# Kernel tuning notes

Measured on AMD Instinct MI355X. Metric: run time of the kernel, lower is better.

Reference implementation:

```python
import jax, jax.numpy as jnp
import numpy as np

B, N, D = 32, 4096, 256
NC, NTPC, NVPT, NS = 16, 8, 4, 16
NT = NC * NTPC          # 128 type codes
NV = NT * NVPT          # 512 variant codes
THRESH = 0.1            # code_sparsity


def setup_inputs() -> dict:
    key = jax.random.key(0)
    ks = jax.random.split(key, 24)
    rn = lambda k, s, sc=0.02: jax.random.normal(k, s, jnp.float32) * sc
    return {
        "X": jax.random.normal(ks[0], (B, N, D), jnp.float32),
        "positions": jax.random.normal(ks[1], (B, N, D), jnp.float32),
        "mask": jnp.ones((B, N), jnp.bool_),
        "category_codes": rn(ks[2], (NC, D)),
        "type_codes": rn(ks[3], (NT, D)),
        "variant_codes": rn(ks[4], (NV, D)),
        "spatial_codes": rn(ks[5], (NS, D)),
        "log_tau": jnp.zeros((1,), jnp.float32),
        "Wk": rn(ks[6], (D, D)), "bk": jnp.zeros((D,), jnp.float32),
        "Wcat": rn(ks[7], (D, D)), "bcat": jnp.zeros((D,), jnp.float32),
        "Wtype": rn(ks[8], (D, D)), "btype": jnp.zeros((D,), jnp.float32),
        "Wvar": rn(ks[9], (D, D)), "bvar": jnp.zeros((D,), jnp.float32),
        "Wsp": rn(ks[10], (D, D)), "bsp": jnp.zeros((D,), jnp.float32),
        "Wg1": rn(ks[11], (D, 2 * D)), "bg1": jnp.zeros((D,), jnp.float32),
        "Wg2": rn(ks[12], (D, D)), "bg2": jnp.zeros((D,), jnp.float32),
        "Wo": rn(ks[13], (D, D)), "bo": jnp.zeros((D,), jnp.float32),
        "ln_g": jnp.ones((D,), jnp.float32), "ln_b": jnp.zeros((D,), jnp.float32),
        "level_weights": jnp.ones((4,), jnp.float32) / 4.0,
    }


def _sparsify(w, thr):
    w = jnp.where(w > thr, w, 0.0)
    return w / (w.sum(-1, keepdims=True) + 1e-8)


def reference(X, positions, mask, category_codes, type_codes, variant_codes,
              spatial_codes, log_tau, Wk, bk, Wcat, bcat, Wtype, btype,
              Wvar, bvar, Wsp, bsp, Wg1, bg1, Wg2, bg2, Wo, bo, ln_g, ln_b,
              level_weights):
    d = X.shape[-1]
    tau = jnp.clip(jnp.exp(log_tau) + 0.1, 0.1, 2.0)  # (1,)
    mv = jnp.finfo(X.dtype).min / 2
    K = X @ Wk.T + bk  # (B,N,d)

    def level(codes, Wq, bq):
        Q = codes @ Wq.T + bq                                    # (M,d)
        attn = jnp.einsum('md,bnd->bmn', Q, K) / jnp.sqrt(jnp.float32(d))
        attn = jnp.where(mask[:, None, :], attn, mv)
        attn = jnp.clip(attn, -50.0, 50.0)
        G = jnp.nan_to_num(jax.nn.softmax(attn, axis=-1))
        H = jnp.einsum('bmn,bnd->bmd', G, X)                     # (B,M,d)
        w_raw = jnp.linalg.norm(H, axis=-1) / tau                # (B,M)
        return H, w_raw

    # level 0: category
    H_cat, w_cat_raw = level(category_codes, Wcat, bcat)
    w_cat_sparse = _sparsify(jax.nn.softmax(w_cat_raw, -1), THRESH)
    # level 1: type (gated by category)
    H_type, w_type_raw = level(type_codes, Wtype, btype)
    w_type_g = (w_type_raw.reshape(-1, NC, NTPC) * w_cat_sparse[:, :, None]).reshape(-1, NT)
    w_type_sparse = _sparsify(jax.nn.softmax(w_type_g, -1), THRESH / 2)
    # level 2: variant (gated by type)
    H_var, w_var_raw = level(variant_codes, Wvar, bvar)
    w_type_exp = jnp.repeat(w_type_sparse, NVPT, axis=-1)        # (B,NV)
    w_var_sparse = _sparsify(jax.nn.softmax(w_var_raw * w_type_exp, -1), THRESH / 4)
    # spatial (independent)
    H_sp, w_sp_raw = level(spatial_codes, Wsp, bsp)
    w_sp_sparse = _sparsify(jax.nn.softmax(w_sp_raw, -1), THRESH)

    z_cat = jnp.einsum('bm,bmd->bd', w_cat_sparse, H_cat)
    z_type = jnp.einsum('bm,bmd->bd', w_type_sparse, H_type)
    z_var = jnp.einsum('bm,bmd->bd', w_var_sparse, H_var)
    z_sp = jnp.einsum('bm,bmd->bd', w_sp_sparse, H_sp)

    lw = jax.nn.softmax(level_weights)
    z = lw[0] * z_cat + lw[1] * z_type + lw[2] * z_var + lw[3] * z_sp

    # position gate: masked mean-pooled positions -> sigmoid gate
    m = mask.astype(X.dtype)
    pos_pool = (positions * m[:, :, None]).sum(1) / (m.sum(1, keepdims=True) + 1e-8)
    h = jax.nn.gelu(jnp.concatenate([z, pos_pool], -1) @ Wg1.T + bg1, approximate=False)
    gate = jax.nn.sigmoid(h @ Wg2.T + bg2)
    z = z * gate

    # out_proj: Linear + LayerNorm
    y = z @ Wo.T + bo
    mu = y.mean(-1, keepdims=True)
    var = ((y - mu) ** 2).mean(-1, keepdims=True)
    y = (y - mu) / jnp.sqrt(var + 1e-5) * ln_g + ln_b
    return y
```

## Files before the change

### kernel.cpp

```cpp
#include <hip/hip_runtime.h>

typedef unsigned short u16;
typedef short v8s __attribute__((ext_vector_type(8)));
typedef float v4f __attribute__((ext_vector_type(4)));

union U16x8 { uint4 u4; v8s s8; u16 us[8]; };

__device__ __forceinline__ u16 f2bf(float x) {
  unsigned int u = __float_as_uint(x);
  u += 0x7fffu + ((u >> 16) & 1u);
  return (u16)(u >> 16);
}

#define GLOBAL_AS __attribute__((address_space(1)))
#define LDS_AS __attribute__((address_space(3)))
__device__ __forceinline__ void async16(const void* g, void* l) {
  __builtin_amdgcn_global_load_lds((const GLOBAL_AS unsigned int*)g,
                                   (LDS_AS unsigned int*)l, 16, 0, 0);
}

#define BB 32
#define NN 4096
#define DD 256
#define M_TOT 672
#define M_PAD 704
#define MT_PER_B 11
#define NSPLIT 4
#define NCHUNK (NN / NSPLIT)

__global__ void kz_zero(float* __restrict__ p, int n) {
  int i = blockIdx.x * 256 + threadIdx.x;
  if (i < n) p[i] = 0.f;
}

__global__ void k0_q(const float* __restrict__ cat, const float* __restrict__ typ,
                     const float* __restrict__ var, const float* __restrict__ spc,
                     const float* __restrict__ Wcat, const float* __restrict__ bcat,
                     const float* __restrict__ Wtype, const float* __restrict__ btype,
                     const float* __restrict__ Wvar, const float* __restrict__ bvar,
                     const float* __restrict__ Wsp, const float* __restrict__ bsp,
                     float* __restrict__ Qall) {
  __shared__ float cl[DD];
  const int m = blockIdx.x, tid = threadIdx.x;
  const float* codes = nullptr; const float* W = nullptr; const float* bia = nullptr; int r = 0;
  if (m < 16)       { codes = cat; r = m;       W = Wcat;  bia = bcat; }
  else if (m < 144) { codes = typ; r = m - 16;  W = Wtype; bia = btype; }
  else if (m < 656) { codes = var; r = m - 144; W = Wvar;  bia = bvar; }
  else if (m < 672) { codes = spc; r = m - 656; W = Wsp;   bia = bsp; }
  cl[tid] = (m < M_TOT) ? codes[r * DD + tid] : 0.f;
  __syncthreads();
  if (m < M_TOT) {
    float acc = bia[tid];
    const float4* w4 = (const float4*)(W + (size_t)tid * DD);
    const float4* c4 = (const float4*)cl;
    #pragma unroll 8
    for (int k = 0; k < 64; ++k) {
      float4 a = c4[k], b = w4[k];
      acc += a.x * b.x + a.y * b.y + a.z * b.z + a.w * b.w;
    }
    Qall[m * DD + tid] = acc;
  } else {
    Qall[m * DD + tid] = 0.f;
  }
}

__global__ void k1_qp(const float* __restrict__ Qall, const float* __restrict__ Wk,
                      const float* __restrict__ bk, u16* __restrict__ Qp,
                      float* __restrict__ qbw) {
  __shared__ float ql[DD];
  __shared__ float red[4];
  const int m = blockIdx.x, tid = threadIdx.x;
  ql[tid] = Qall[m * DD + tid];
  __syncthreads();
  float acc = 0.f;
  for (int j = 0; j < DD; ++j) acc += ql[j] * Wk[(size_t)j * DD + tid];
  Qp[m * DD + tid] = f2bf(acc);
  float p = ql[tid] * bk[tid];
  #pragma unroll
  for (int off = 32; off > 0; off >>= 1) p += __shfl_down(p, off, 64);
  if ((tid & 63) == 0) red[tid >> 6] = p;
  __syncthreads();
  if (tid == 0) qbw[m] = red[0] + red[1] + red[2] + red[3];
}

__global__ void k2_cast(const float* __restrict__ X, u16* __restrict__ Xb,
                        u16* __restrict__ XbT) {
  __shared__ u16 tl[64][72];
  const int n0 = blockIdx.x * 64, d0 = blockIdx.y * 64, b = blockIdx.z;
  const int tid = threadIdx.x;
  const int nl = tid >> 4, d4 = tid & 15;
  #pragma unroll
  for (int rr = 0; rr < 4; ++rr) {
    const int n = n0 + nl + rr * 16;
    float4 v = *(const float4*)(X + ((size_t)b * NN + n) * DD + d0 + d4 * 4);
    ushort4 h;
    h.x = f2bf(v.x); h.y = f2bf(v.y); h.z = f2bf(v.z); h.w = f2bf(v.w);
    *(ushort4*)(Xb + ((size_t)b * NN + n) * DD + d0 +
                (((d4 >> 1) ^ (n & 7)) << 3) + (d4 & 1) * 4) = h;
    *(ushort4*)(&tl[nl + rr * 16][d4 * 4]) = h;
  }
  __syncthreads();
  const int dl = tid >> 4, n4 = tid & 15;
  #pragma unroll
  for (int rr = 0; rr < 4; ++rr) {
    const int d = dl + rr * 16;
    ushort4 h;
    h.x = tl[n4 * 4 + 0][d]; h.y = tl[n4 * 4 + 1][d];
    h.z = tl[n4 * 4 + 2][d]; h.w = tl[n4 * 4 + 3][d];
    *(ushort4*)(XbT + ((size_t)b * DD + d0 + d) * NN + n0 +
                (((n4 >> 1) ^ (dl & 7)) << 3) + (n4 & 1) * 4) = h;
  }
}

__global__ __launch_bounds__(256, 2) void pf_fused(
    const u16* __restrict__ Xb, const u16* __restrict__ XbT,
    const u16* __restrict__ Qp, const float* __restrict__ qbw,
    const unsigned char* __restrict__ mask,
    float* __restrict__ HP, float* __restrict__ sumsP) {
  __shared__ u16 sX[64 * 256];
  __shared__ u16 sXT[256 * 64];
  __shared__ u16 sP[64 * 64];

  const int id = blockIdx.x;
  const int xcd = id & 7, lin = id >> 3;
  const int ggl = lin / MT_PER_B, k = lin - ggl * MT_PER_B;
  const int gg = xcd * 16 + ggl;
  const int b = gg >> 2, split = gg & 3;
  const int m0 = k * 64;
  const int ns0 = split * NCHUNK;

  const int tid = threadIdx.x;
  const int lane = tid & 63, w = tid >> 6;
  const int q = lane >> 4, c16 = lane & 15;
  const int wmQ = (w >> 1) * 32, wn = (w & 1) * 32;
  const int wd = w * 64;

  v8s aq[2][4][2];
  #pragma unroll
  for (int mi = 0; mi < 2; ++mi) {
    const u16* qrow = Qp + (size_t)(m0 + wmQ + mi * 16 + c16) * DD;
    #pragma unroll
    for (int ks = 0; ks < 4; ++ks)
      #pragma unroll
      for (int kk = 0; kk < 2; ++kk) {
        U16x8 u; u.u4 = *(const uint4*)(qrow + ks * 64 + kk * 32 + q * 8);
        aq[mi][ks][kk] = u.s8;
      }
  }
  float qv[2][4];
  #pragma unroll
  for (int mi = 0; mi < 2; ++mi)
    #pragma unroll
    for (int r = 0; r < 4; ++r)
      qv[mi][r] = qbw[m0 + wmQ + mi * 16 + q * 4 + r];

  v4f hacc[4][4];
  #pragma unroll
  for (int mi = 0; mi < 4; ++mi)
    #pragma unroll
    for (int di = 0; di < 4; ++di) hacc[mi][di] = (v4f){0.f, 0.f, 0.f, 0.f};
  float rs[2][4];
  #pragma unroll
  for (int mi = 0; mi < 2; ++mi)
    #pragma unroll
    for (int r = 0; r < 4; ++r) rs[mi][r] = 0.f;

  const u16* XbB = Xb + (size_t)b * NN * DD;
  const u16* XTB = XbT + (size_t)b * DD * NN;
  const unsigned char* mkB = mask + (size_t)b * NN;

  for (int it = 0; it < NCHUNK / 64; ++it) {
    const int n0g = ns0 + it * 64;
    __syncthreads();
    #pragma unroll
    for (int i = 0; i < 8; ++i) {
      const int c = i * 256 + tid;
      async16(XbB + (size_t)(n0g + (c >> 5)) * DD + (c & 31) * 8, sX + c * 8);
    }
    #pragma unroll
    for (int i = 0; i < 8; ++i) {
      const int c = i * 256 + tid;
      async16(XTB + (size_t)(c >> 3) * NN + n0g + (c & 7) * 8, sXT + c * 8);
    }
    __syncthreads();

    v4f sacc[2][2];
    #pragma unroll
    for (int mi = 0; mi < 2; ++mi)
      #pragma unroll
      for (int ni = 0; ni < 2; ++ni) sacc[mi][ni] = (v4f){0.f, 0.f, 0.f, 0.f};
    #pragma unroll
    for (int ks = 0; ks < 4; ++ks)
      #pragma unroll
      for (int kk = 0; kk < 2; ++kk) {
        v8s bq[2];
        #pragma unroll
        for (int ni = 0; ni < 2; ++ni) {
          const int n = wn + ni * 16 + c16;
          U16x8 u;
          u.u4 = *(const uint4*)(sX + n * 256 + (((ks * 8 + kk * 4 + q) ^ (n & 7)) << 3));
          bq[ni] = u.s8;
        }
        #pragma unroll
        for (int mi = 0; mi < 2; ++mi)
          #pragma unroll
          for (int ni = 0; ni < 2; ++ni)
            sacc[mi][ni] = __builtin_amdgcn_mfma_f32_16x16x32_bf16(
                aq[mi][ks][kk], bq[ni], sacc[mi][ni], 0, 0, 0);
      }

    #pragma unroll
    for (int ni = 0; ni < 2; ++ni) {
      const int nl = wn + ni * 16 + c16;
      const bool mk = mkB[n0g + nl] != 0;
      #pragma unroll
      for (int mi = 0; mi < 2; ++mi)
        #pragma unroll
        for (int r = 0; r < 4; ++r) {
          float s = (sacc[mi][ni][r] + qv[mi][r]) * 0.0625f;
          s = fminf(fmaxf(s, -50.f), 50.f);
          s = mk ? s : -50.f;
          float p = __expf(s);
          rs[mi][r] += p;
          const int ml = wmQ + mi * 16 + q * 4 + r;
          sP[ml * 64 + (nl ^ ((ml & 7) << 3))] = f2bf(p);
        }
    }
    __syncthreads();

    #pragma unroll
    for (int kk = 0; kk < 2; ++kk) {
      v8s pa[4];
      #pragma unroll
      for (int mi = 0; mi < 4; ++mi) {
        const int ml = mi * 16 + c16;
        U16x8 u;
        u.u4 = *(const uint4*)(sP + ml * 64 + ((kk * 32 + q * 8) ^ ((ml & 7) << 3)));
        pa[mi] = u.s8;
      }
      #pragma unroll
      for (int di = 0; di < 4; ++di) {
        const int d = wd + di * 16 + c16;
        U16x8 u;
        u.u4 = *(const uint4*)(sXT + d * 64 + (((kk * 4 + q) ^ (d & 7)) << 3));
        #pragma unroll
        for (int mi = 0; mi < 4; ++mi)
          hacc[mi][di] = __builtin_amdgcn_mfma_f32_16x16x32_bf16(
              pa[mi], u.s8, hacc[mi][di], 0, 0, 0);
      }
    }
  }

  float* HPb = HP + ((size_t)split * BB + b) * M_PAD * DD;
  #pragma unroll
  for (int mi = 0; mi < 4; ++mi)
    #pragma unroll
    for (int di = 0; di < 4; ++di)
      #pragma unroll
      for (int r = 0; r < 4; ++r) {
        const int m = m0 + mi * 16 + q * 4 + r;
        HPb[(size_t)m * DD + wd + di * 16 + c16] = hacc[mi][di][r];
      }

  __syncthreads();
  float* fred = (float*)sP;
  #pragma unroll
  for (int mi = 0; mi < 2; ++mi)
    #pragma unroll
    for (int r = 0; r < 4; ++r) {
      float v = rs[mi][r];
      v += __shfl_xor(v, 1, 64);
      v += __shfl_xor(v, 2, 64);
      v += __shfl_xor(v, 4, 64);
      v += __shfl_xor(v, 8, 64);
      if (c16 == 0) fred[(w & 1) * 64 + wmQ + mi * 16 + q * 4 + r] = v;
    }
  __syncthreads();
  if (tid < 64) {
    sumsP[((size_t)split * BB + b) * M_PAD + m0 + tid] = fred[tid] + fred[64 + tid];
  }
}

__global__ void khr_reduce(float* __restrict__ HP, const float* __restrict__ sumsP,
                           float* __restrict__ sums, float* __restrict__ nrm) {
  __shared__ float red[64][4];
  const int mt = blockIdx.x, b = blockIdx.y, tid = threadIdx.x;
  const int lane = tid & 63, w = tid >> 6;
  const int m0 = mt * 64;
  const size_t SP = (size_t)BB * M_PAD * DD;
  float* base = HP + ((size_t)b * M_PAD + m0) * DD;
  for (int mi = 0; mi < 64; ++mi) {
    const size_t idx = (size_t)mi * DD + tid;
    float h = base[idx] + base[idx + SP] + base[idx + 2 * SP] + base[idx + 3 * SP];
    base[idx] = h;
    float v = h * h;
    v += __shfl_xor(v, 1, 64);
    v += __shfl_xor(v, 2, 64);
    v += __shfl_xor(v, 4, 64);
    v += __shfl_xor(v, 8, 64);
    v += __shfl_xor(v, 16, 64);
    v += __shfl_xor(v, 32, 64);
    if (lane == 0) red[mi][w] = v;
  }
  __syncthreads();
  if (tid < 64) {
    const size_t o = (size_t)b * M_PAD + m0 + tid;
    nrm[o] = red[tid][0] + red[tid][1] + red[tid][2] + red[tid][3];
    const size_t ss = (size_t)BB * M_PAD;
    const size_t si = (size_t)b * M_PAD + m0 + tid;
    sums[o] = sumsP[si] + sumsP[si + ss] + sumsP[si + 2 * ss] + sumsP[si + 3 * ss];
  }
}

__global__ void k4_pool(const float* __restrict__ pos, const unsigned char* __restrict__ mask,
                        float* __restrict__ pp, float* __restrict__ cnt) {
  __shared__ float sp[4][256];
  __shared__ float sc[4];
  const int cx = blockIdx.x, b = blockIdx.y, tid = threadIdx.x;
  const int nl = tid >> 6, d4 = tid & 63;
  const int n0 = cx * 256;
  float4 acc = {0.f, 0.f, 0.f, 0.f};
  float c = 0.f;
  for (int i = 0; i < 64; ++i) {
    const int n = n0 + i * 4 + nl;
    const float m = mask[(size_t)b * NN + n] ? 1.f : 0.f;
    c += m;
    float4 v = *(const float4*)(pos + ((size_t)b * NN + n) * DD + d4 * 4);
    acc.x += m * v.x; acc.y += m * v.y; acc.z += m * v.z; acc.w += m * v.w;
  }
  *(float4*)(&sp[nl][d4 * 4]) = acc;
  if (d4 == 0) sc[nl] = c;
  __syncthreads();
  pp[((size_t)b * 16 + cx) * DD + tid] = sp[0][tid] + sp[1][tid] + sp[2][tid] + sp[3][tid];
  if (tid == 0) cnt[b * 16 + cx] = sc[0] + sc[1] + sc[2] + sc[3];
}

__device__ void softmax_sparsify(const float* in, int nn, float* outp, float thr) {
  float mx = -3.4e38f;
  for (int i = 0; i < nn; ++i) mx = fmaxf(mx, in[i]);
  float s = 0.f;
  for (int i = 0; i < nn; ++i) { float e = __expf(in[i] - mx); outp[i] = e; s += e; }
  float s2 = 0.f;
  for (int i = 0; i < nn; ++i) {
    float v = outp[i] / s;
    v = (v > thr) ? v : 0.f;
    outp[i] = v; s2 += v;
  }
  const float inv = 1.f / (s2 + 1e-8f);
  for (int i = 0; i < nn; ++i) outp[i] *= inv;
}

__global__ void k5a_weights(const float* __restrict__ nrm, const float* __restrict__ sums,
                            const float* __restrict__ log_tau,
                            const float* __restrict__ lvlw, float* __restrict__ wbufG) {
  __shared__ float wr[M_TOT];
  __shared__ float wcat[16], wtyp[128], wvar[512], wsp[16], lw[4];
  __shared__ float tmp[128];
  const int b = blockIdx.x, tid = threadIdx.x;
  const float tau = fminf(fmaxf(__expf(log_tau[0]) + 0.1f, 0.1f), 2.0f);
  for (int m = tid; m < M_TOT; m += 256)
    wr[m] = sqrtf(nrm[(size_t)b * M_PAD + m]) / (sums[(size_t)b * M_PAD + m] * tau);
  __syncthreads();
  if (tid == 0) {
    softmax_sparsify(wr, 16, wcat, 0.1f);
    for (int i = 0; i < 128; ++i) tmp[i] = wr[16 + i] * wcat[i >> 3];
    softmax_sparsify(tmp, 128, wtyp, 0.05f);
    for (int i = 0; i < 512; ++i) wvar[i] = wr[144 + i] * wtyp[i >> 2];
    softmax_sparsify(wvar, 512, wvar, 0.025f);
    softmax_sparsify(wr + 656, 16, wsp, 0.1f);
    float mx = fmaxf(fmaxf(lvlw[0], lvlw[1]), fmaxf(lvlw[2], lvlw[3]));
    float s = 0.f;
    for (int i = 0; i < 4; ++i) { lw[i] = __expf(lvlw[i] - mx); s += lw[i]; }
    for (int i = 0; i < 4; ++i) lw[i] /= s;
  }
  __syncthreads();
  for (int m = tid; m < M_TOT; m += 256) {
    float v;
    if (m < 16)       v = lw[0] * wcat[m];
    else if (m < 144) v = lw[1] * wtyp[m - 16];
    else if (m < 656) v = lw[2] * wvar[m - 144];
    else              v = lw[3] * wsp[m - 656];
    wbufG[(size_t)b * M_PAD + m] = v / sums[(size_t)b * M_PAD + m];
  }
}

__global__ void k5b_z(const float* __restrict__ Hws, const float* __restrict__ wbufG,
                      float* __restrict__ zacc) {
  const int mc = blockIdx.x, b = blockIdx.y, tid = threadIdx.x;
  const float* Hb = Hws + (size_t)b * M_PAD * DD;
  const float* wb = wbufG + (size_t)b * M_PAD;
  float acc = 0.f;
  #pragma unroll 4
  for (int i = 0; i < 84; ++i) {
    const int m = mc * 84 + i;
    acc += wb[m] * Hb[(size_t)m * DD + tid];
  }
  atomicAdd(&zacc[(size_t)b * DD + tid], acc);
}

__global__ void k5c_mlp(const float* __restrict__ zacc, const float* __restrict__ pp,
                        const float* __restrict__ cnt,
                        const float* __restrict__ Wg1, const float* __restrict__ bg1,
                        const float* __restrict__ Wg2, const float* __restrict__ bg2,
                        const float* __restrict__ Wo, const float* __restrict__ bo,
                        const float* __restrict__ lng, const float* __restrict__ lnb,
                        float* __restrict__ out) {
  __shared__ float zb[DD], pb[DD], hb[DD], zg[DD];
  __shared__ float red[8];
  const int b = blockIdx.x, tid = threadIdx.x;
  const int lane = tid & 63, w = tid >> 6;

  float p = 0.f, c = 0.f;
  for (int ch = 0; ch < 16; ++ch) {
    p += pp[((size_t)b * 16 + ch) * DD + tid];
    c += cnt[b * 16 + ch];
  }
  zb[tid] = zacc[(size_t)b * DD + tid];
  pb[tid] = p / (c + 1e-8f);
  __syncthreads();

  float h = bg1[tid];
  {
    const float4* w4 = (const float4*)(Wg1 + (size_t)tid * 512);
    const float4* z4 = (const float4*)zb;
    const float4* p4 = (const float4*)pb;
    for (int k = 0; k < 64; ++k) {
      float4 a = z4[k], bb = w4[k];
      h += a.x * bb.x + a.y * bb.y + a.z * bb.z + a.w * bb.w;
    }
    for (int k = 0; k < 64; ++k) {
      float4 a = p4[k], bb = w4[64 + k];
      h += a.x * bb.x + a.y * bb.y + a.z * bb.z + a.w * bb.w;
    }
  }
  h = 0.5f * h * (1.f + erff(h * 0.70710678118654752f));
  hb[tid] = h;
  __syncthreads();

  float g = bg2[tid];
  {
    const float4* w4 = (const float4*)(Wg2 + (size_t)tid * DD);
    const float4* h4 = (const float4*)hb;
    for (int k = 0; k < 64; ++k) {
      float4 a = h4[k], bb = w4[k];
      g += a.x * bb.x + a.y * bb.y + a.z * bb.z + a.w * bb.w;
    }
  }
  g = 1.f / (1.f + __expf(-g));
  zg[tid] = zb[tid] * g;
  __syncthreads();

  float y = bo[tid];
  {
    const float4* w4 = (const float4*)(Wo + (size_t)tid * DD);
    const float4* z4 = (const float4*)zg;
    for (int k = 0; k < 64; ++k) {
      float4 a = z4[k], bb = w4[k];
      y += a.x * bb.x + a.y * bb.y + a.z * bb.z + a.w * bb.w;
    }
  }

  float s = y;
  #pragma unroll
  for (int off = 32; off > 0; off >>= 1) s += __shfl_xor(s, off, 64);
  if (lane == 0) red[w] = s;
  __syncthreads();
  const float mu = (red[0] + red[1] + red[2] + red[3]) * (1.f / 256.f);
  float dv = (y - mu) * (y - mu);
  #pragma unroll
  for (int off = 32; off > 0; off >>= 1) dv += __shfl_xor(dv, off, 64);
  if (lane == 0) red[4 + w] = dv;
  __syncthreads();
  const float var = (red[4] + red[5] + red[6] + red[7]) * (1.f / 256.f);
  out[(size_t)b * DD + tid] = (y - mu) / sqrtf(var + 1e-5f) * lng[tid] + lnb[tid];
}

extern "C" void kernel_launch(void* const* d_in, const int* in_sizes, int n_in,
                              void* d_out, int out_size, void* d_ws, size_t ws_size,
                              hipStream_t stream) {
  const float* X          = (const float*)d_in[0];
  const float* positions  = (const float*)d_in[1];
  const unsigned char* mask = (const unsigned char*)d_in[2];
  const float* cat  = (const float*)d_in[3];
  const float* typ  = (const float*)d_in[4];
  const float* var  = (const float*)d_in[5];
  const float* spc  = (const float*)d_in[6];
  const float* log_tau = (const float*)d_in[7];
  const float* Wk   = (const float*)d_in[8];   const float* bk    = (const float*)d_in[9];
  const float* Wcat = (const float*)d_in[10];  const float* bcat  = (const float*)d_in[11];
  const float* Wtype= (const float*)d_in[12];  const float* btype = (const float*)d_in[13];
  const float* Wvar = (const float*)d_in[14];  const float* bvar  = (const float*)d_in[15];
  const float* Wsp  = (const float*)d_in[16];  const float* bsp   = (const float*)d_in[17];
  const float* Wg1  = (const float*)d_in[18];  const float* bg1   = (const float*)d_in[19];
  const float* Wg2  = (const float*)d_in[20];  const float* bg2   = (const float*)d_in[21];
  const float* Wo   = (const float*)d_in[22];  const float* bo    = (const float*)d_in[23];
  const float* lng  = (const float*)d_in[24];  const float* lnb   = (const float*)d_in[25];
  const float* lvlw = (const float*)d_in[26];

  char* ws = (char*)d_ws;
  size_t off = 0;
  auto alloc = [&](size_t bytes) { size_t o = off; off = (off + bytes + 255) & ~255ULL; return o; };
  const size_t oXb   = alloc((size_t)BB * NN * DD * 2);
  const size_t oXT   = alloc((size_t)BB * DD * NN * 2);
  const size_t oQall = alloc((size_t)M_PAD * DD * 4);
  const size_t oQp   = alloc((size_t)M_PAD * DD * 2);
  const size_t oQb   = alloc((size_t)M_PAD * 4);
  const size_t oSums = alloc((size_t)BB * M_PAD * 4);
  const size_t oSumsP= alloc((size_t)NSPLIT * BB * M_PAD * 4);
  const size_t oNrm  = alloc((size_t)BB * M_PAD * 4);
  const size_t oZac  = alloc((size_t)BB * DD * 4);
  const size_t oWbf  = alloc((size_t)BB * M_PAD * 4);
  const size_t oHP   = alloc((size_t)NSPLIT * BB * M_PAD * DD * 4);
  const size_t oPP   = alloc((size_t)BB * 16 * DD * 4);
  const size_t oCNT  = alloc((size_t)BB * 16 * 4);

  u16*   Xb   = (u16*)(ws + oXb);
  u16*   XbT  = (u16*)(ws + oXT);
  float* Qall = (float*)(ws + oQall);
  u16*   Qp   = (u16*)(ws + oQp);
  float* qbw  = (float*)(ws + oQb);
  float* sums = (float*)(ws + oSums);
  float* sumsP= (float*)(ws + oSumsP);
  float* nrm  = (float*)(ws + oNrm);
  float* zacc = (float*)(ws + oZac);
  float* wbfG = (float*)(ws + oWbf);
  float* HP   = (float*)(ws + oHP);
  float* ppw  = (float*)(ws + oPP);
  float* cntw = (float*)(ws + oCNT);

  const int nzero = BB * DD;
  kz_zero<<<(nzero + 255) / 256, 256, 0, stream>>>(zacc, nzero);
  k0_q<<<M_PAD, 256, 0, stream>>>(cat, typ, var, spc, Wcat, bcat, Wtype, btype,
                                  Wvar, bvar, Wsp, bsp, Qall);
  k1_qp<<<M_PAD, 256, 0, stream>>>(Qall, Wk, bk, Qp, qbw);
  k2_cast<<<dim3(64, 4, 32), 256, 0, stream>>>(X, Xb, XbT);
  k4_pool<<<dim3(16, 32), 256, 0, stream>>>(positions, mask, ppw, cntw);
  pf_fused<<<dim3(BB * MT_PER_B * NSPLIT), 256, 0, stream>>>(Xb, XbT, Qp, qbw, mask,
                                                             HP, sumsP);
  khr_reduce<<<dim3(MT_PER_B, BB), 256, 0, stream>>>(HP, sumsP, sums, nrm);
  k5a_weights<<<32, 256, 0, stream>>>(nrm, sums, log_tau, lvlw, wbfG);
  k5b_z<<<dim3(8, 32), 256, 0, stream>>>(HP, wbfG, zacc);
  k5c_mlp<<<32, 256, 0, stream>>>(zacc, ppw, cntw, Wg1, bg1, Wg2, bg2, Wo, bo,
                                  lng, lnb, (float*)d_out);
}
```

Before: 736.3 us.

## Register-prefetch next X tile in main kernel, fuse Q kernels, drop z atomics

The main attention kernel stops using direct global-to-LDS async loads. It now loads the next 64-row X and X-transposed tiles into registers while the current tile is computed, then writes them to LDS at the start of the next iteration. Separately, the two query-projection kernels are merged into one so the Qall buffer round trip goes away. The zero-init kernel and the atomic z accumulation are replaced by per-chunk partial sums that the MLP kernel adds up. The register prefetch adds 16 uint4 registers per thread, which may reduce occupancy of a kernel that already holds large accumulator arrays.

```diff
diff --git a/kernel.cpp b/kernel.cpp
--- a/kernel.cpp
+++ b/kernel.cpp
@@ -10,13 +10,6 @@
   unsigned int u = __float_as_uint(x);
   u += 0x7fffu + ((u >> 16) & 1u);
   return (u16)(u >> 16);
-}
-
-#define GLOBAL_AS __attribute__((address_space(1)))
-#define LDS_AS __attribute__((address_space(3)))
-__device__ __forceinline__ void async16(const void* g, void* l) {
-  __builtin_amdgcn_global_load_lds((const GLOBAL_AS unsigned int*)g,
-                                   (LDS_AS unsigned int*)l, 16, 0, 0);
 }
 
 #define BB 32
@@ -28,19 +21,17 @@
 #define NSPLIT 4
 #define NCHUNK (NN / NSPLIT)
 
-__global__ void kz_zero(float* __restrict__ p, int n) {
-  int i = blockIdx.x * 256 + threadIdx.x;
-  if (i < n) p[i] = 0.f;
-}
-
-__global__ void k0_q(const float* __restrict__ cat, const float* __restrict__ typ,
-                     const float* __restrict__ var, const float* __restrict__ spc,
-                     const float* __restrict__ Wcat, const float* __restrict__ bcat,
-                     const float* __restrict__ Wtype, const float* __restrict__ btype,
-                     const float* __restrict__ Wvar, const float* __restrict__ bvar,
-                     const float* __restrict__ Wsp, const float* __restrict__ bsp,
-                     float* __restrict__ Qall) {
+__global__ void k01_q(const float* __restrict__ cat, const float* __restrict__ typ,
+                      const float* __restrict__ var, const float* __restrict__ spc,
+                      const float* __restrict__ Wcat, const float* __restrict__ bcat,
+                      const float* __restrict__ Wtype, const float* __restrict__ btype,
+                      const float* __restrict__ Wvar, const float* __restrict__ bvar,
+                      const float* __restrict__ Wsp, const float* __restrict__ bsp,
+                      const float* __restrict__ Wk, const float* __restrict__ bk,
+                      u16* __restrict__ Qp, float* __restrict__ qbw) {
   __shared__ float cl[DD];
+  __shared__ float ql[DD];
+  __shared__ float red[4];
   const int m = blockIdx.x, tid = threadIdx.x;
   const float* codes = nullptr; const float* W = nullptr; const float* bia = nullptr; int r = 0;
   if (m < 16)       { codes = cat; r = m;       W = Wcat;  bia = bcat; }
@@ -49,8 +40,9 @@
   else if (m < 672) { codes = spc; r = m - 656; W = Wsp;   bia = bsp; }
   cl[tid] = (m < M_TOT) ? codes[r * DD + tid] : 0.f;
   __syncthreads();
+  float acc = 0.f;
   if (m < M_TOT) {
-    float acc = bia[tid];
+    acc = bia[tid];
     const float4* w4 = (const float4*)(W + (size_t)tid * DD);
     const float4* c4 = (const float4*)cl;
     #pragma unroll 8
@@ -58,23 +50,12 @@
       float4 a = c4[k], b = w4[k];
       acc += a.x * b.x + a.y * b.y + a.z * b.z + a.w * b.w;
     }
-    Qall[m * DD + tid] = acc;
-  } else {
-    Qall[m * DD + tid] = 0.f;
-  }
-}
-
-__global__ void k1_qp(const float* __restrict__ Qall, const float* __restrict__ Wk,
-                      const float* __restrict__ bk, u16* __restrict__ Qp,
-                      float* __restrict__ qbw) {
-  __shared__ float ql[DD];
-  __shared__ float red[4];
-  const int m = blockIdx.x, tid = threadIdx.x;
-  ql[tid] = Qall[m * DD + tid];
-  __syncthreads();
-  float acc = 0.f;
-  for (int j = 0; j < DD; ++j) acc += ql[j] * Wk[(size_t)j * DD + tid];
-  Qp[m * DD + tid] = f2bf(acc);
+  }
+  ql[tid] = acc;
+  __syncthreads();
+  float acc2 = 0.f;
+  for (int j = 0; j < DD; ++j) acc2 += ql[j] * Wk[(size_t)j * DD + tid];
+  Qp[m * DD + tid] = f2bf(acc2);
   float p = ql[tid] * bk[tid];
   #pragma unroll
   for (int off = 32; off > 0; off >>= 1) p += __shfl_down(p, off, 64);
@@ -135,6 +116,21 @@
   const int wmQ = (w >> 1) * 32, wn = (w & 1) * 32;
   const int wd = w * 64;
 
+  const u16* XbB = Xb + (size_t)b * NN * DD;
+  const u16* XTB = XbT + (size_t)b * DD * NN;
+  const unsigned char* mkB = mask + (size_t)b * NN;
+
+  uint4 rx[8], rt[8];
+  {
+    const int n0g = ns0;
+    #pragma unroll
+    for (int i = 0; i < 8; ++i) {
+      const int c = i * 256 + tid;
+      rx[i] = *(const uint4*)(XbB + (size_t)(n0g + (c >> 5)) * DD + (c & 31) * 8);
+      rt[i] = *(const uint4*)(XTB + (size_t)(c >> 3) * NN + n0g + (c & 7) * 8);
+    }
+  }
+
   v8s aq[2][4][2];
   #pragma unroll
   for (int mi = 0; mi < 2; ++mi) {
@@ -165,22 +161,23 @@
     #pragma unroll
     for (int r = 0; r < 4; ++r) rs[mi][r] = 0.f;
 
-  const u16* XbB = Xb + (size_t)b * NN * DD;
-  const u16* XTB = XbT + (size_t)b * DD * NN;
-  const unsigned char* mkB = mask + (size_t)b * NN;
-
   for (int it = 0; it < NCHUNK / 64; ++it) {
     const int n0g = ns0 + it * 64;
     __syncthreads();
     #pragma unroll
     for (int i = 0; i < 8; ++i) {
       const int c = i * 256 + tid;
-      async16(XbB + (size_t)(n0g + (c >> 5)) * DD + (c & 31) * 8, sX + c * 8);
-    }
-    #pragma unroll
-    for (int i = 0; i < 8; ++i) {
-      const int c = i * 256 + tid;
-      async16(XTB + (size_t)(c >> 3) * NN + n0g + (c & 7) * 8, sXT + c * 8);
+      *(uint4*)(sX + c * 8) = rx[i];
+      *(uint4*)(sXT + c * 8) = rt[i];
+    }
+    if (it < NCHUNK / 64 - 1) {
+      const int n1g = n0g + 64;
+      #pragma unroll
+      for (int i = 0; i < 8; ++i) {
+        const int c = i * 256 + tid;
+        rx[i] = *(const uint4*)(XbB + (size_t)(n1g + (c >> 5)) * DD + (c & 31) * 8);
+        rt[i] = *(const uint4*)(XTB + (size_t)(c >> 3) * NN + n1g + (c & 7) * 8);
+      }
     }
     __syncthreads();
 
@@ -385,7 +382,7 @@
 }
 
 __global__ void k5b_z(const float* __restrict__ Hws, const float* __restrict__ wbufG,
-                      float* __restrict__ zacc) {
+                      float* __restrict__ zaccP) {
   const int mc = blockIdx.x, b = blockIdx.y, tid = threadIdx.x;
   const float* Hb = Hws + (size_t)b * M_PAD * DD;
   const float* wb = wbufG + (size_t)b * M_PAD;
@@ -395,10 +392,10 @@
     const int m = mc * 84 + i;
     acc += wb[m] * Hb[(size_t)m * DD + tid];
   }
-  atomicAdd(&zacc[(size_t)b * DD + tid], acc);
-}
-
-__global__ void k5c_mlp(const float* __restrict__ zacc, const float* __restrict__ pp,
+  zaccP[((size_t)mc * BB + b) * DD + tid] = acc;
+}
+
+__global__ void k5c_mlp(const float* __restrict__ zaccP, const float* __restrict__ pp,
                         const float* __restrict__ cnt,
                         const float* __restrict__ Wg1, const float* __restrict__ bg1,
                         const float* __restrict__ Wg2, const float* __restrict__ bg2,
@@ -415,7 +412,10 @@
     p += pp[((size_t)b * 16 + ch) * DD + tid];
     c += cnt[b * 16 + ch];
   }
-  zb[tid] = zacc[(size_t)b * DD + tid];
+  float z = 0.f;
+  for (int ch = 0; ch < 8; ++ch)
+    z += zaccP[((size_t)ch * BB + b) * DD + tid];
+  zb[tid] = z;
   pb[tid] = p / (c + 1e-8f);
   __syncthreads();
 
@@ -502,13 +502,12 @@
   auto alloc = [&](size_t bytes) { size_t o = off; off = (off + bytes + 255) & ~255ULL; return o; };
   const size_t oXb   = alloc((size_t)BB * NN * DD * 2);
   const size_t oXT   = alloc((size_t)BB * DD * NN * 2);
-  const size_t oQall = alloc((size_t)M_PAD * DD * 4);
   const size_t oQp   = alloc((size_t)M_PAD * DD * 2);
   const size_t oQb   = alloc((size_t)M_PAD * 4);
   const size_t oSums = alloc((size_t)BB * M_PAD * 4);
   const size_t oSumsP= alloc((size_t)NSPLIT * BB * M_PAD * 4);
   const size_t oNrm  = alloc((size_t)BB * M_PAD * 4);
-  const size_t oZac  = alloc((size_t)BB * DD * 4);
+  const size_t oZacP = alloc((size_t)8 * BB * DD * 4);
   const size_t oWbf  = alloc((size_t)BB * M_PAD * 4);
   const size_t oHP   = alloc((size_t)NSPLIT * BB * M_PAD * DD * 4);
   const size_t oPP   = alloc((size_t)BB * 16 * DD * 4);
@@ -516,30 +515,26 @@
 
   u16*   Xb   = (u16*)(ws + oXb);
   u16*   XbT  = (u16*)(ws + oXT);
-  float* Qall = (float*)(ws + oQall);
   u16*   Qp   = (u16*)(ws + oQp);
   float* qbw  = (float*)(ws + oQb);
   float* sums = (float*)(ws + oSums);
   float* sumsP= (float*)(ws + oSumsP);
   float* nrm  = (float*)(ws + oNrm);
-  float* zacc = (float*)(ws + oZac);
+  float* zaccP= (float*)(ws + oZacP);
   float* wbfG = (float*)(ws + oWbf);
   float* HP   = (float*)(ws + oHP);
   float* ppw  = (float*)(ws + oPP);
   float* cntw = (float*)(ws + oCNT);
 
-  const int nzero = BB * DD;
-  kz_zero<<<(nzero + 255) / 256, 256, 0, stream>>>(zacc, nzero);
-  k0_q<<<M_PAD, 256, 0, stream>>>(cat, typ, var, spc, Wcat, bcat, Wtype, btype,
-                                  Wvar, bvar, Wsp, bsp, Qall);
-  k1_qp<<<M_PAD, 256, 0, stream>>>(Qall, Wk, bk, Qp, qbw);
+  k01_q<<<M_PAD, 256, 0, stream>>>(cat, typ, var, spc, Wcat, bcat, Wtype, btype,
+                                   Wvar, bvar, Wsp, bsp, Wk, bk, Qp, qbw);
   k2_cast<<<dim3(64, 4, 32), 256, 0, stream>>>(X, Xb, XbT);
   k4_pool<<<dim3(16, 32), 256, 0, stream>>>(positions, mask, ppw, cntw);
   pf_fused<<<dim3(BB * MT_PER_B * NSPLIT), 256, 0, stream>>>(Xb, XbT, Qp, qbw, mask,
                                                              HP, sumsP);
   khr_reduce<<<dim3(MT_PER_B, BB), 256, 0, stream>>>(HP, sumsP, sums, nrm);
   k5a_weights<<<32, 256, 0, stream>>>(nrm, sums, log_tau, lvlw, wbfG);
-  k5b_z<<<dim3(8, 32), 256, 0, stream>>>(HP, wbfG, zacc);
-  k5c_mlp<<<32, 256, 0, stream>>>(zacc, ppw, cntw, Wg1, bg1, Wg2, bg2, Wo, bo,
+  k5b_z<<<dim3(8, 32), 256, 0, stream>>>(HP, wbfG, zaccP);
+  k5c_mlp<<<32, 256, 0, stream>>>(zaccP, ppw, cntw, Wg1, bg1, Wg2, bg2, Wo, bo,
                                   lng, lnb, (float*)d_out);
 }
```

Result: slower. 1.473 ms (+100.0%).
